# Kernel optimization log

Measured on AMD Instinct MI355X. Metric: run time of the kernel, lower is better.

The kernel has to match this reference:

```python
import jax, jax.numpy as jnp
import numpy as np

B, N, U, K = 2, 768, 64, 8
IN = 2 * U + K  # 136
SLOPE = 0.01    # torch LeakyReLU default


def setup_inputs() -> dict:
    key = jax.random.key(0)
    ks = jax.random.split(key, 12)
    seq_embed = jax.random.normal(ks[0], (B, N, U), dtype=jnp.float32)
    vals = jax.random.uniform(ks[1], (N, N, K), dtype=jnp.float32)
    edge = (jax.random.uniform(ks[2], (N, N)) < 0.05) | jnp.eye(N, dtype=bool)
    relational_encoding = vals * edge[:, :, None].astype(jnp.float32)
    s = 0.05
    inp = {"seq_embed": seq_embed, "relational_encoding": relational_encoding}
    # per-hop MLP params: hop k has Linear(IN,IN) then Linear(IN,1); W stored (in,out)
    inp["w1_1"] = jax.random.normal(ks[3], (IN, IN), dtype=jnp.float32) * s
    inp["b1_1"] = jax.random.normal(ks[4], (IN,), dtype=jnp.float32) * s
    inp["w1_2"] = jax.random.normal(ks[5], (IN, 1), dtype=jnp.float32) * s
    inp["b1_2"] = jax.random.normal(ks[6], (1,), dtype=jnp.float32) * s
    inp["w2_1"] = jax.random.normal(ks[7], (IN, IN), dtype=jnp.float32) * s
    inp["b2_1"] = jax.random.normal(ks[8], (IN,), dtype=jnp.float32) * s
    inp["w2_2"] = jax.random.normal(ks[9], (IN, 1), dtype=jnp.float32) * s
    inp["b2_2"] = jax.random.normal(ks[10], (1,), dtype=jnp.float32) * s
    return inp


def _fwd(seq_embed, relational_encoding, hop_params):
    mask = (relational_encoding.sum(-1) > 0).astype(seq_embed.dtype)  # (N,N)
    D = mask.sum(-1)  # (N,) row degree
    rel = relational_encoding[None]  # (1,N,N,K) broadcast over batch
    x = seq_embed
    for layers in hop_params:
        b, n, u = x.shape
        e_i = jnp.broadcast_to(x[:, :, None, :], (b, n, n, u))  # row embed
        e_j = jnp.broadcast_to(x[:, None, :, :], (b, n, n, u))  # col embed
        seq_combined = jnp.concatenate([e_i, e_j], axis=-1)     # (B,N,N,2U)
        combined = jnp.concatenate(
            [seq_combined, jnp.broadcast_to(rel, (b, n, n, rel.shape[-1]))], axis=-1)
        combined = combined * mask[None, :, :, None]
        w = combined
        for (W, bb) in layers:
            w = jax.nn.leaky_relu(w @ W + bb, SLOPE)
        w = w[..., 0] * mask[None]                 # (B,N,N)
        scaled = w / D[None, :, None]              # divide each row i by D[i]
        # weighted neighbor embeds = scaled * e_j, summed over dim 1 (rows)
        x = jnp.einsum('bij,biju->bju', scaled, e_j)
    return x


def reference(seq_embed, relational_encoding, w1_1, b1_1, w1_2, b1_2,
              w2_1, b2_1, w2_2, b2_2):
    hop_params = [[(w1_1, b1_1), (w1_2, b1_2)], [(w2_1, b2_1), (w2_2, b2_2)]]
    return _fwd(seq_embed, relational_encoding, hop_params)
```

## Files before the change

### kernel.cpp

```cpp
#include <hip/hip_runtime.h>

#define NN 768
#define UU 64
#define KK 8
#define INF 136
#define BB 2
#define SLOPE 0.01f
#define RECCAP 61440
#define NP 16
#define PSTRIDE 1552

__device__ __forceinline__ float lrelu(float x) { return x > 0.f ? x : SLOPE * x; }


__device__ __forceinline__ float sum_copies(const float* __restrict__ sp, int bj) {
    float f = 0.f;
#pragma unroll
    for (int p = 0; p < NP; p++) f += sp[p * PSTRIDE + bj];
    return f;
}

__device__ __forceinline__ void pre_rows(int r4base, const float* __restrict__ x,
                                         const float* __restrict__ sc,
                                         const float* __restrict__ W1,
                                         float* __restrict__ A, float* __restrict__ Bv,
                                         float (*xs)[UU], int tid) {
    {
        int rr = tid >> 6, u = tid & 63;
        int bi = r4base + rr;
        float f = sc ? sum_copies(sc, bi) : 1.0f;
        xs[rr][u] = x[(size_t)bi * UU + u] * f;
    }
    __syncthreads();
    int m = tid;
    if (m < INF) {
        float a[4] = {0.f, 0.f, 0.f, 0.f}, bv[4] = {0.f, 0.f, 0.f, 0.f};
        for (int u = 0; u < UU; u++) {
            float wa = W1[u * INF + m];
            float wb = W1[(UU + u) * INF + m];
#pragma unroll
            for (int r = 0; r < 4; r++) {
                a[r]  += xs[r][u] * wa;
                bv[r] += xs[r][u] * wb;
            }
        }
#pragma unroll
        for (int r = 0; r < 4; r++) {
            A [(size_t)(r4base + r) * INF + m] = a[r];
            Bv[(size_t)(r4base + r) * INF + m] = bv[r];
        }
    }
}

__global__ void __launch_bounds__(256) k_fused0(
        const float* __restrict__ rel, const float* __restrict__ seq,
        const float* __restrict__ W1, int* __restrict__ recs,
        float* __restrict__ dinv, int* __restrict__ gcount,
        float* __restrict__ A, float* __restrict__ Bv) {
    __shared__ float xs[4][UU];
    __shared__ int wcnt[4];
    __shared__ int sbase;
    int blk = blockIdx.x;
    int tid = threadIdx.x;

    if (blk >= NN) {
        pre_rows((blk - NN) * 4, seq, nullptr, W1, A, Bv, xs, tid);
        return;
    }

    int i = blk;
    int w = tid >> 6, lane = tid & 63;
    int j0 = w * 192;
    float sums[3];
#pragma unroll
    for (int it = 0; it < 3; it++) {
        int j = j0 + it * 64 + lane;
        const float4* rp = (const float4*)(rel + (size_t)(i * NN + j) * KK);
        float4 a = rp[0], b = rp[1];
        sums[it] = a.x + a.y + a.z + a.w + b.x + b.y + b.z + b.w;
    }
    int cnt = 0;
    int pos[3];
    bool act[3];
#pragma unroll
    for (int it = 0; it < 3; it++) {
        act[it] = sums[it] > 0.f;
        unsigned long long m = __ballot(act[it]);
        pos[it] = cnt + __popcll(m & ((1ull << lane) - 1));
        cnt += __popcll(m);
    }
    if (lane == 0) wcnt[w] = cnt;
    __syncthreads();
    int prefix = 0, total = 0;
#pragma unroll
    for (int ww = 0; ww < 4; ww++) {
        int c = wcnt[ww];
        total += c;
        if (ww < w) prefix += c;
    }
    if (tid == 0) {
        sbase = atomicAdd(gcount, total);
        dinv[i] = 1.0f / (float)total;
    }
    __syncthreads();
    int base = sbase;
#pragma unroll
    for (int it = 0; it < 3; it++) {
        if (act[it]) {
            int rp = base + prefix + pos[it];
            if (rp < RECCAP) recs[rp] = (i << 16) | (j0 + it * 64 + lane);
        }
    }
}

__global__ void __launch_bounds__(256) k_pre(const float* __restrict__ x,
                                             const float* __restrict__ sc,
                                             const float* __restrict__ W1,
                                             float* __restrict__ A, float* __restrict__ Bv) {
    __shared__ float xs[4][UU];
    pre_rows(blockIdx.x * 4, x, sc, W1, A, Bv, xs, threadIdx.x);
}

__global__ void __launch_bounds__(256) k_hop(
        const int* __restrict__ recs, const int* __restrict__ gcount,
        const float* __restrict__ A, const float* __restrict__ Bv,
        const float* __restrict__ rel, const float* __restrict__ W1,
        const float* __restrict__ b1, const float* __restrict__ w2,
        const float* __restrict__ b2, const float* __restrict__ dinv,
        float* __restrict__ sp) {
    int lane = threadIdx.x & 63;
    int wid = (blockIdx.x * blockDim.x + threadIdx.x) >> 6;
    int cnt = *gcount;
    int p = wid * 4;
    if (p >= cnt) return;
    float* s = sp + (wid & (NP - 1)) * PSTRIDE;

    const float* W1R = W1 + 128 * INF;
    float w1r0[8], w1r1[8], w1r2[8];
#pragma unroll
    for (int k = 0; k < 8; k++) {
        w1r0[k] = W1R[k * INF + lane];
        w1r1[k] = W1R[k * INF + 64 + lane];
        w1r2[k] = W1R[k * INF + 128 + (lane & 7)];
    }
    float b10 = b1[lane], b11 = b1[64 + lane], b12 = b1[128 + (lane & 7)];
    float w20 = w2[lane], w21 = w2[64 + lane];
    float w22 = (lane < 8) ? w2[128 + lane] : 0.f;
    float b2v = b2[0];

    int4 q = *(const int4*)(recs + p);
    int rr4[4] = {q.x, q.y, q.z, q.w};

#pragma unroll
    for (int t = 0; t < 4; t++) {
        if (p + t >= cnt) break;
        int rec = rr4[t];
        int i = rec >> 16, j = rec & 0xffff;
        const float* relp = rel + (size_t)(i * NN + j) * KK;
        float4 ra = ((const float4*)relp)[0];
        float4 rb = ((const float4*)relp)[1];
        float di = dinv[i];
        float rv[8] = {ra.x, ra.y, ra.z, ra.w, rb.x, rb.y, rb.z, rb.w};
        float r0 = b10, r1 = b11, r2 = b12;
#pragma unroll
        for (int k = 0; k < 8; k++) {
            r0 += rv[k] * w1r0[k];
            r1 += rv[k] * w1r1[k];
            r2 += rv[k] * w1r2[k];
        }
        float dd[BB];
#pragma unroll
        for (int b = 0; b < BB; b++) {
            const float* Ai = A  + ((size_t)b * NN + i) * INF;
            const float* Bj = Bv + ((size_t)b * NN + j) * INF;
            float dot = lrelu(r0 + Ai[lane]      + Bj[lane])      * w20
                      + lrelu(r1 + Ai[64 + lane] + Bj[64 + lane]) * w21;
            if (lane < 8)
                dot += lrelu(r2 + Ai[128 + lane] + Bj[128 + lane]) * w22;
#pragma unroll
            for (int off = 32; off; off >>= 1) dot += __shfl_xor(dot, off, 64);
            dd[b] = dot;
        }
        if (lane == 0)  atomicAdd(&s[j],      lrelu(dd[0] + b2v) * di);
        if (lane == 32) atomicAdd(&s[NN + j], lrelu(dd[1] + b2v) * di);
    }
}

__global__ void __launch_bounds__(256) k_final(const float4* __restrict__ seq,
                                               const float* __restrict__ s1p,
                                               const float* __restrict__ s2p,
                                               float4* __restrict__ out) {
    int idx = blockIdx.x * blockDim.x + threadIdx.x;
    int bj = idx >> 4;
    float f = sum_copies(s1p, bj) * sum_copies(s2p, bj);
    float4 v = seq[idx];
    v.x *= f; v.y *= f; v.z *= f; v.w *= f;
    out[idx] = v;
}

extern "C" void kernel_launch(void* const* d_in, const int* in_sizes, int n_in,
                              void* d_out, int out_size, void* d_ws, size_t ws_size,
                              hipStream_t stream) {
    const float* seq = (const float*)d_in[0];
    const float* rel = (const float*)d_in[1];
    const float* w1_1 = (const float*)d_in[2];
    const float* b1_1 = (const float*)d_in[3];
    const float* w1_2 = (const float*)d_in[4];
    const float* b1_2 = (const float*)d_in[5];
    const float* w2_1 = (const float*)d_in[6];
    const float* b2_1 = (const float*)d_in[7];
    const float* w2_2 = (const float*)d_in[8];
    const float* b2_2 = (const float*)d_in[9];
    float* out = (float*)d_out;

    char* ws = (char*)d_ws;
    float* s1p    = (float*)(ws + 0);
    float* s2p    = (float*)(ws + 99328);
    int*   gcount = (int*)  (ws + 198656);
    float* dinv   = (float*)(ws + 198912);
    float* A      = (float*)(ws + 202752);
    float* Bv     = (float*)(ws + 1038336);
    int*   recs   = (int*)  (ws + 1873920);

    hipMemsetAsync(ws, 0, 198660, stream);

    k_fused0<<<NN + 384, 256, 0, stream>>>(rel, seq, w1_1, recs, dinv, gcount, A, Bv);

    k_hop<<<RECCAP / 16, 256, 0, stream>>>(recs, gcount, A, Bv, rel, w1_1, b1_1, w1_2, b1_2, dinv, s1p);

    k_pre<<<384, 256, 0, stream>>>(seq, s1p, w2_1, A, Bv);
    k_hop<<<RECCAP / 16, 256, 0, stream>>>(recs, gcount, A, Bv, rel, w2_1, b2_1, w2_2, b2_2, dinv, s2p);

    k_final<<<BB * NN * UU / 4 / 256, 256, 0, stream>>>((const float4*)seq, s1p, s2p, (float4*)out);
}
```

Baseline: 145.2 us.

## Pack row scale into edge records and software-pipeline gathers in hop kernel

Each edge record becomes an int2 that carries the row's 1/degree alongside the packed (i,j), so the separate dinv array and its dependent load go away. The last-finishing block of the scan pads the record list to a multiple of four with zero-weight entries, which lets the hop kernel drop its per-record bounds check. The hop kernel loads all A/B/rel operands for a pair before computing an earlier one, giving several gathers in flight per wave, and adds an occupancy hint to launch bounds. The cost is higher register pressure, a doubled record footprint, and a grid-wide completion counter with thread fences.

```diff
diff --git a/kernel.cpp b/kernel.cpp
--- a/kernel.cpp
+++ b/kernel.cpp
@@ -54,8 +54,8 @@
 
 __global__ void __launch_bounds__(256) k_fused0(
         const float* __restrict__ rel, const float* __restrict__ seq,
-        const float* __restrict__ W1, int* __restrict__ recs,
-        float* __restrict__ dinv, int* __restrict__ gcount,
+        const float* __restrict__ W1, int2* __restrict__ recs,
+        int* __restrict__ gcount, int* __restrict__ done, int* __restrict__ gpad,
         float* __restrict__ A, float* __restrict__ Bv) {
     __shared__ float xs[4][UU];
     __shared__ int wcnt[4];
@@ -98,17 +98,27 @@
         total += c;
         if (ww < w) prefix += c;
     }
-    if (tid == 0) {
-        sbase = atomicAdd(gcount, total);
-        dinv[i] = 1.0f / (float)total;
-    }
+    if (tid == 0) sbase = atomicAdd(gcount, total);
     __syncthreads();
     int base = sbase;
+    float di = 1.0f / (float)total;
 #pragma unroll
     for (int it = 0; it < 3; it++) {
         if (act[it]) {
             int rp = base + prefix + pos[it];
-            if (rp < RECCAP) recs[rp] = (i << 16) | (j0 + it * 64 + lane);
+            if (rp < RECCAP)
+                recs[rp] = make_int2((i << 16) | (j0 + it * 64 + lane), __float_as_int(di));
+        }
+    }
+    if (tid == 0) {
+        __threadfence();
+        int od = atomicAdd(done, 1);
+        if (od == NN - 1) {
+            __threadfence();
+            int c = atomicAdd(gcount, 0);
+            int pad = (c + 3) & ~3;
+            for (int t = c; t < pad; t++) recs[t] = make_int2(0, 0);
+            *gpad = pad;
         }
     }
 }
@@ -121,18 +131,72 @@
     pre_rows(blockIdx.x * 4, x, sc, W1, A, Bv, xs, threadIdx.x);
 }
 
-__global__ void __launch_bounds__(256) k_hop(
-        const int* __restrict__ recs, const int* __restrict__ gcount,
+struct PairLoad {
+    float4 ra, rb;
+    float av[BB][3], bvv[BB][3];
+    float di;
+    int j;
+};
+
+__device__ __forceinline__ void load_pair(PairLoad& P, int2 rec, int lane,
+                                          const float* __restrict__ A,
+                                          const float* __restrict__ Bv,
+                                          const float* __restrict__ rel) {
+    int ij = rec.x;
+    int i = ij >> 16, j = ij & 0xffff;
+    P.j = j;
+    P.di = __int_as_float(rec.y);
+    const float* relp = rel + (size_t)(i * NN + j) * KK;
+    P.ra = ((const float4*)relp)[0];
+    P.rb = ((const float4*)relp)[1];
+#pragma unroll
+    for (int b = 0; b < BB; b++) {
+        const float* Ai = A  + ((size_t)b * NN + i) * INF;
+        const float* Bj = Bv + ((size_t)b * NN + j) * INF;
+        P.av[b][0] = Ai[lane]; P.av[b][1] = Ai[64 + lane]; P.av[b][2] = Ai[128 + (lane & 7)];
+        P.bvv[b][0] = Bj[lane]; P.bvv[b][1] = Bj[64 + lane]; P.bvv[b][2] = Bj[128 + (lane & 7)];
+    }
+}
+
+__device__ __forceinline__ void compute_pair(const PairLoad& P, int lane,
+                                             const float* w1r0, const float* w1r1,
+                                             const float* w1r2,
+                                             float b10, float b11, float b12,
+                                             float w20, float w21, float w22, float b2v,
+                                             float* __restrict__ s) {
+    float rv[8] = {P.ra.x, P.ra.y, P.ra.z, P.ra.w, P.rb.x, P.rb.y, P.rb.z, P.rb.w};
+    float r0 = b10, r1 = b11, r2 = b12;
+#pragma unroll
+    for (int k = 0; k < 8; k++) {
+        r0 += rv[k] * w1r0[k];
+        r1 += rv[k] * w1r1[k];
+        r2 += rv[k] * w1r2[k];
+    }
+    float dd[BB];
+#pragma unroll
+    for (int b = 0; b < BB; b++) {
+        float dot = lrelu(r0 + P.av[b][0] + P.bvv[b][0]) * w20
+                  + lrelu(r1 + P.av[b][1] + P.bvv[b][1]) * w21;
+        if (lane < 8)
+            dot += lrelu(r2 + P.av[b][2] + P.bvv[b][2]) * w22;
+#pragma unroll
+        for (int off = 32; off; off >>= 1) dot += __shfl_xor(dot, off, 64);
+        dd[b] = dot;
+    }
+    if (lane == 0)  atomicAdd(&s[P.j],      lrelu(dd[0] + b2v) * P.di);
+    if (lane == 32) atomicAdd(&s[NN + P.j], lrelu(dd[1] + b2v) * P.di);
+}
+
+__global__ void __launch_bounds__(256, 6) k_hop(
+        const int2* __restrict__ recs, const int* __restrict__ gpad,
         const float* __restrict__ A, const float* __restrict__ Bv,
         const float* __restrict__ rel, const float* __restrict__ W1,
         const float* __restrict__ b1, const float* __restrict__ w2,
-        const float* __restrict__ b2, const float* __restrict__ dinv,
-        float* __restrict__ sp) {
+        const float* __restrict__ b2, float* __restrict__ sp) {
     int lane = threadIdx.x & 63;
     int wid = (blockIdx.x * blockDim.x + threadIdx.x) >> 6;
-    int cnt = *gcount;
     int p = wid * 4;
-    if (p >= cnt) return;
+    if (p >= *gpad) return;
     float* s = sp + (wid & (NP - 1)) * PSTRIDE;
 
     const float* W1R = W1 + 128 * INF;
@@ -148,42 +212,18 @@
     float w22 = (lane < 8) ? w2[128 + lane] : 0.f;
     float b2v = b2[0];
 
-    int4 q = *(const int4*)(recs + p);
-    int rr4[4] = {q.x, q.y, q.z, q.w};
-
-#pragma unroll
-    for (int t = 0; t < 4; t++) {
-        if (p + t >= cnt) break;
-        int rec = rr4[t];
-        int i = rec >> 16, j = rec & 0xffff;
-        const float* relp = rel + (size_t)(i * NN + j) * KK;
-        float4 ra = ((const float4*)relp)[0];
-        float4 rb = ((const float4*)relp)[1];
-        float di = dinv[i];
-        float rv[8] = {ra.x, ra.y, ra.z, ra.w, rb.x, rb.y, rb.z, rb.w};
-        float r0 = b10, r1 = b11, r2 = b12;
-#pragma unroll
-        for (int k = 0; k < 8; k++) {
-            r0 += rv[k] * w1r0[k];
-            r1 += rv[k] * w1r1[k];
-            r2 += rv[k] * w1r2[k];
-        }
-        float dd[BB];
-#pragma unroll
-        for (int b = 0; b < BB; b++) {
-            const float* Ai = A  + ((size_t)b * NN + i) * INF;
-            const float* Bj = Bv + ((size_t)b * NN + j) * INF;
-            float dot = lrelu(r0 + Ai[lane]      + Bj[lane])      * w20
-                      + lrelu(r1 + Ai[64 + lane] + Bj[64 + lane]) * w21;
-            if (lane < 8)
-                dot += lrelu(r2 + Ai[128 + lane] + Bj[128 + lane]) * w22;
-#pragma unroll
-            for (int off = 32; off; off >>= 1) dot += __shfl_xor(dot, off, 64);
-            dd[b] = dot;
-        }
-        if (lane == 0)  atomicAdd(&s[j],      lrelu(dd[0] + b2v) * di);
-        if (lane == 32) atomicAdd(&s[NN + j], lrelu(dd[1] + b2v) * di);
-    }
+    int4 qa = *(const int4*)(recs + p);
+    int4 qb = *(const int4*)(recs + p + 2);
+
+    PairLoad P0, P1, P2, P3;
+    load_pair(P0, make_int2(qa.x, qa.y), lane, A, Bv, rel);
+    load_pair(P1, make_int2(qa.z, qa.w), lane, A, Bv, rel);
+    load_pair(P2, make_int2(qb.x, qb.y), lane, A, Bv, rel);
+    compute_pair(P0, lane, w1r0, w1r1, w1r2, b10, b11, b12, w20, w21, w22, b2v, s);
+    load_pair(P3, make_int2(qb.z, qb.w), lane, A, Bv, rel);
+    compute_pair(P1, lane, w1r0, w1r1, w1r2, b10, b11, b12, w20, w21, w22, b2v, s);
+    compute_pair(P2, lane, w1r0, w1r1, w1r2, b10, b11, b12, w20, w21, w22, b2v, s);
+    compute_pair(P3, lane, w1r0, w1r1, w1r2, b10, b11, b12, w20, w21, w22, b2v, s);
 }
 
 __global__ void __launch_bounds__(256) k_final(const float4* __restrict__ seq,
@@ -217,19 +257,20 @@
     float* s1p    = (float*)(ws + 0);
     float* s2p    = (float*)(ws + 99328);
     int*   gcount = (int*)  (ws + 198656);
-    float* dinv   = (float*)(ws + 198912);
+    int*   done   = (int*)  (ws + 198660);
+    int*   gpad   = (int*)  (ws + 198664);
     float* A      = (float*)(ws + 202752);
     float* Bv     = (float*)(ws + 1038336);
-    int*   recs   = (int*)  (ws + 1873920);
-
-    hipMemsetAsync(ws, 0, 198660, stream);
-
-    k_fused0<<<NN + 384, 256, 0, stream>>>(rel, seq, w1_1, recs, dinv, gcount, A, Bv);
-
-    k_hop<<<RECCAP / 16, 256, 0, stream>>>(recs, gcount, A, Bv, rel, w1_1, b1_1, w1_2, b1_2, dinv, s1p);
+    int2*  recs   = (int2*) (ws + 1873920);
+
+    hipMemsetAsync(ws, 0, 198668, stream);
+
+    k_fused0<<<NN + 384, 256, 0, stream>>>(rel, seq, w1_1, recs, gcount, done, gpad, A, Bv);
+
+    k_hop<<<RECCAP / 16, 256, 0, stream>>>(recs, gpad, A, Bv, rel, w1_1, b1_1, w1_2, b1_2, s1p);
 
     k_pre<<<384, 256, 0, stream>>>(seq, s1p, w2_1, A, Bv);
-    k_hop<<<RECCAP / 16, 256, 0, stream>>>(recs, gcount, A, Bv, rel, w2_1, b2_1, w2_2, b2_2, dinv, s2p);
+    k_hop<<<RECCAP / 16, 256, 0, stream>>>(recs, gpad, A, Bv, rel, w2_1, b2_1, w2_2, b2_2, s2p);
 
     k_final<<<BB * NN * UU / 4 / 256, 256, 0, stream>>>((const float4*)seq, s1p, s2p, (float4*)out);
 }
```

Measured after the change: 201.4 us. 1.39x slower.
